# Kernel tuning notes

Hardware: AMD Instinct MI355X
Metric: run time of the kernel (lower is better)

## Reference

```python
import jax, jax.numpy as jnp
import numpy as np

N = 50000
E = 800000
IN = 64
HID = 64
OUT = 32
R = 8
B = 8
EPS = 1e-5


def setup_inputs() -> dict:
    key = jax.random.key(0)
    ks = jax.random.split(key, 20)
    s_in = 1.0 / np.sqrt(IN)
    s_hid = 1.0 / np.sqrt(HID)
    inp = {
        "x": jax.random.normal(ks[0], (N, IN), dtype=jnp.float32),
        "edge_index": jax.random.randint(ks[1], (2, E), 0, N, dtype=jnp.int64) if jax.config.jax_enable_x64 else jax.random.randint(ks[1], (2, E), 0, N),
        "edge_type": jax.random.randint(ks[2], (E,), 0, R),
        # conv1: in -> hid
        "comp1": jax.random.normal(ks[3], (R, B), dtype=jnp.float32) * (1.0 / np.sqrt(B)),
        "bases1": jax.random.normal(ks[4], (B, IN, HID), dtype=jnp.float32) * s_in,
        "root1": jax.random.normal(ks[5], (IN, HID), dtype=jnp.float32) * s_in,
        "bias1": jnp.zeros((HID,), dtype=jnp.float32),
        # conv2 (hidden): hid -> hid
        "comp2": jax.random.normal(ks[6], (R, B), dtype=jnp.float32) * (1.0 / np.sqrt(B)),
        "bases2": jax.random.normal(ks[7], (B, HID, HID), dtype=jnp.float32) * s_hid,
        "root2": jax.random.normal(ks[8], (HID, HID), dtype=jnp.float32) * s_hid,
        "bias2": jnp.zeros((HID,), dtype=jnp.float32),
        # conv_out: hid -> out
        "comp3": jax.random.normal(ks[9], (R, B), dtype=jnp.float32) * (1.0 / np.sqrt(B)),
        "bases3": jax.random.normal(ks[10], (B, HID, OUT), dtype=jnp.float32) * s_hid,
        "root3": jax.random.normal(ks[11], (HID, OUT), dtype=jnp.float32) * s_hid,
        "bias3": jnp.zeros((OUT,), dtype=jnp.float32),
        # batchnorms
        "gamma1": jnp.ones((HID,), dtype=jnp.float32),
        "beta1": jnp.zeros((HID,), dtype=jnp.float32),
        "gamma2": jnp.ones((HID,), dtype=jnp.float32),
        "beta2": jnp.zeros((HID,), dtype=jnp.float32),
    }
    return inp


def rgcn_conv(x, src, dst, etype, comp, bases, root, bias):
    """PyG-style RGCNConv with basis decomposition and per-relation mean aggregation."""
    n = x.shape[0]
    # project node features through all bases: [N, B, O]
    xb = jnp.einsum('ni,bio->nbo', x, bases)
    # per-edge relation coefficients [E, B] contract with gathered basis features [E, B, O]
    msg = jnp.einsum('eb,ebo->eo', comp[etype], xb[src])
    # mean normalization per (dst node, relation)
    seg = dst * R + etype
    cnt = jax.ops.segment_sum(jnp.ones((msg.shape[0],), dtype=x.dtype), seg, num_segments=n * R)
    msg = msg / jnp.maximum(cnt[seg], 1.0)[:, None]
    agg = jax.ops.segment_sum(msg, dst, num_segments=n)
    return agg + x @ root + bias


def batch_norm(x, gamma, beta):
    mu = jnp.mean(x, axis=0)
    var = jnp.mean(jnp.square(x - mu), axis=0)  # biased, as torch BN training
    return (x - mu) * jax.lax.rsqrt(var + EPS) * gamma + beta


def reference(x, edge_index, edge_type, comp1, bases1, root1, bias1,
              comp2, bases2, root2, bias2, comp3, bases3, root3, bias3,
              gamma1, beta1, gamma2, beta2):
    src, dst = edge_index[0], edge_index[1]
    h = rgcn_conv(x, src, dst, edge_type, comp1, bases1, root1, bias1)
    h = batch_norm(jax.nn.relu(h), gamma1, beta1)  # dropout = identity (eval)
    h_res = h  # residual since in_channels == hidden_channels
    h2 = rgcn_conv(h, src, dst, edge_type, comp2, bases2, root2, bias2)
    h2 = batch_norm(jax.nn.relu(h2), gamma2, beta2)
    h = h2 + h_res
    out = rgcn_conv(h, src, dst, edge_type, comp3, bases3, root3, bias3)
    return out
```

## Files before the change

kernel.cpp:

```cpp
#include <hip/hip_runtime.h>

#define NN 50000
#define NE 800000
#define RR 8
#define BB 8
#define EPSV 1e-5f
#define SCAN_B ((NN + 255) / 256)

typedef unsigned short bfu;
typedef __attribute__((ext_vector_type(8))) short bf16x8;
typedef __attribute__((ext_vector_type(4))) float f32x4;

__device__ inline float bf2f(bfu u) { return __uint_as_float(((unsigned)u) << 16); }
__device__ inline bfu f2bf(float f) {
    unsigned u = __float_as_uint(f);
    return (bfu)((u + 0x7fffu + ((u >> 16) & 1u)) >> 16);
}

__global__ void zero_f32(float* __restrict__ p, long n) {
    long i = (long)blockIdx.x * blockDim.x + threadIdx.x;
    long stride = (long)gridDim.x * blockDim.x;
    for (; i < n; i += stride) p[i] = 0.f;
}

__global__ void cvt_bf16(const float* __restrict__ x, bfu* __restrict__ xb, long n) {
    long i = (long)blockIdx.x * blockDim.x + threadIdx.x;
    long stride = (long)gridDim.x * blockDim.x;
    for (; i < n; i += stride) xb[i] = f2bf(x[i]);
}

__global__ void build_w_packed(const float* __restrict__ comp, const float* __restrict__ bases,
                               const float* __restrict__ root, bfu* __restrict__ Wp, int O) {
    int idx = blockIdx.x * blockDim.x + threadIdx.x;
    int tot = 576 * O;
    if (idx >= tot) return;
    int k = idx / O, o = idx % O;
    float val;
    if (k < 512) {
        int r = k >> 6, i = k & 63;
        val = 0.f;
#pragma unroll
        for (int b = 0; b < BB; ++b)
            val += comp[r * BB + b] * bases[(b * 64 + i) * O + o];
    } else {
        val = root[(k - 512) * O + o];
    }
    int kt = k >> 5, kk = k & 31;
    int lane = ((kk >> 3) << 4) | (o & 15);
    int pos = ((kt * (O / 16) + (o >> 4)) * 64 + lane) * 8 + (kk & 7);
    Wp[pos] = f2bf(val);
}

__global__ void edge_count(const int* __restrict__ ei, const int* __restrict__ et,
                           float* __restrict__ cnt) {
    int i = blockIdx.x * blockDim.x + threadIdx.x;
    int stride = gridDim.x * blockDim.x;
    for (int e = i; e < NE; e += stride) {
        int d = ei[NE + e];
        int r = et[e];
        atomicAdd(&cnt[(size_t)d * RR + r], 1.0f);
    }
}

__global__ void scan1(const float* __restrict__ cnt, int* __restrict__ offs, int* __restrict__ bsum) {
    __shared__ int sh[256];
    int b = blockIdx.x, t = threadIdx.x;
    int i = b * 256 + t;
    int v = 0;
    if (i < NN) {
        float s = 0.f;
#pragma unroll
        for (int r = 0; r < RR; ++r) s += cnt[(size_t)i * RR + r];
        v = (int)s;
    }
    sh[t] = v;
    __syncthreads();
    for (int s = 1; s < 256; s <<= 1) {
        int tmp = (t >= s) ? sh[t - s] : 0;
        __syncthreads();
        sh[t] += tmp;
        __syncthreads();
    }
    if (i < NN) offs[i] = sh[t] - v;
    if (t == 255) bsum[b] = sh[255];
}

__global__ void scan2(int* __restrict__ bsum, int* __restrict__ offs) {
    if (threadIdx.x == 0 && blockIdx.x == 0) {
        int run = 0;
        for (int b = 0; b < SCAN_B; ++b) { int t = bsum[b]; bsum[b] = run; run += t; }
        offs[NN] = run;
    }
}

__global__ void scan3(int* __restrict__ offs, const int* __restrict__ bsum) {
    int b = blockIdx.x, t = threadIdx.x;
    int i = b * 256 + t;
    if (i < NN) offs[i] += bsum[b];
}

__global__ void place(const int* __restrict__ ei, const int* __restrict__ et,
                      const int* __restrict__ offs, int* __restrict__ fill,
                      unsigned* __restrict__ esrt) {
    int i = blockIdx.x * blockDim.x + threadIdx.x;
    int stride = gridDim.x * blockDim.x;
    for (int e = i; e < NE; e += stride) {
        int d = ei[NE + e];
        int pos = offs[d] + atomicAdd(&fill[d], 1);
        esrt[pos] = ((unsigned)ei[e] << 3) | (unsigned)et[e];
    }
}

#define ACCUM(U, V)                                              \
    switch (__builtin_amdgcn_readfirstlane((int)((U) & 7u))) {   \
        case 0: a0 += (V); break;                                \
        case 1: a1 += (V); break;                                \
        case 2: a2 += (V); break;                                \
        case 3: a3 += (V); break;                                \
        case 4: a4 += (V); break;                                \
        case 5: a5 += (V); break;                                \
        case 6: a6 += (V); break;                                \
        default: a7 += (V); break;                               \
    }

template <int O, bool RELU>
__global__ __launch_bounds__(256) void agg_gemm(const int* __restrict__ offs,
                                                const unsigned* __restrict__ esrt,
                                                const float* __restrict__ cnt,
                                                const bfu* __restrict__ xb,
                                                const bfu* __restrict__ Wp,
                                                const float* __restrict__ bias,
                                                float* __restrict__ outp) {
    constexpr int CT = O / 16;
    __shared__ bfu Af[1152 * 8];
    int wave = threadIdx.x >> 6, lane = threadIdx.x & 63;
    int n0 = blockIdx.x * 16;
    int c = lane;
    int swz_lo = ((c >> 3) & 3) << 4;

#pragma unroll 1
    for (int i = 0; i < 4; ++i) {
        int row = wave * 4 + i;
        int n = n0 + row;
        int j0 = offs[n], j1 = offs[n + 1];
        float a0 = 0.f, a1 = 0.f, a2 = 0.f, a3 = 0.f, a4 = 0.f, a5 = 0.f, a6 = 0.f, a7 = 0.f;
        int j = j0;
        for (; j + 4 <= j1; j += 4) {
            unsigned u0 = esrt[j], u1 = esrt[j + 1], u2 = esrt[j + 2], u3 = esrt[j + 3];
            float v0 = bf2f(xb[(size_t)(u0 >> 3) * 64 + lane]);
            float v1 = bf2f(xb[(size_t)(u1 >> 3) * 64 + lane]);
            float v2 = bf2f(xb[(size_t)(u2 >> 3) * 64 + lane]);
            float v3 = bf2f(xb[(size_t)(u3 >> 3) * 64 + lane]);
            ACCUM(u0, v0); ACCUM(u1, v1); ACCUM(u2, v2); ACCUM(u3, v3);
        }
        for (; j < j1; ++j) {
            unsigned u = esrt[j];
            float v = bf2f(xb[(size_t)(u >> 3) * 64 + lane]);
            ACCUM(u, v);
        }
#define WR(r, ar) {                                                            \
        float inv = 1.f / fmaxf(cnt[(size_t)n * RR + (r)], 1.f);               \
        bfu bv = f2bf((ar) * inv);                                             \
        int g = (2 * (r) + (c >> 5)) * 64 + (row | swz_lo);                    \
        int gs = g ^ ((g >> 3) & 7) ^ ((g >> 6) & 7);                          \
        Af[gs * 8 + (c & 7)] = bv; }
        WR(0, a0) WR(1, a1) WR(2, a2) WR(3, a3)
        WR(4, a4) WR(5, a5) WR(6, a6) WR(7, a7)
#undef WR
        {
            bfu bv = xb[(size_t)n * 64 + lane];
            int g = (16 + (c >> 5)) * 64 + (row | swz_lo);
            int gs = g ^ ((g >> 3) & 7) ^ ((g >> 6) & 7);
            Af[gs * 8 + (c & 7)] = bv;
        }
    }
    __syncthreads();

    int ct = wave;
    if (CT == 4 || ct < CT) {
        f32x4 acc = (f32x4){0.f, 0.f, 0.f, 0.f};
#pragma unroll
        for (int kt = 0; kt < 18; ++kt) {
            int g = kt * 64 + lane;
            int gs = g ^ ((g >> 3) & 7) ^ ((g >> 6) & 7);
            bf16x8 af = *(const bf16x8*)&Af[gs * 8];
            bf16x8 bfv = *(const bf16x8*)&Wp[((size_t)(kt * CT + ct) * 64 + lane) * 8];
            acc = __builtin_amdgcn_mfma_f32_16x16x32_bf16(af, bfv, acc, 0, 0, 0);
        }
        int col = ct * 16 + (lane & 15);
        float b = bias[col];
#pragma unroll
        for (int jj = 0; jj < 4; ++jj) {
            int row = (lane >> 4) * 4 + jj;
            float v = acc[jj] + b;
            if (RELU) v = fmaxf(v, 0.f);
            outp[(size_t)(n0 + row) * O + col] = v;
        }
    }
}

__global__ void bn_stats(const float* __restrict__ y, float* __restrict__ stats) {
    int c = threadIdx.x & 63;
    int rg = threadIdx.x >> 6;
    float s = 0.f, q = 0.f;
    for (int n = blockIdx.x * 4 + rg; n < NN; n += gridDim.x * 4) {
        float v = y[(size_t)n * 64 + c];
        s += v;
        q += v * v;
    }
    __shared__ float ls[4][64], lq[4][64];
    ls[rg][c] = s;
    lq[rg][c] = q;
    __syncthreads();
    if (rg == 0) {
        s = ls[0][c] + ls[1][c] + ls[2][c] + ls[3][c];
        q = lq[0][c] + lq[1][c] + lq[2][c] + lq[3][c];
        atomicAdd(&stats[c], s);
        atomicAdd(&stats[64 + c], q);
    }
}

__global__ void bn_finalize(const float* __restrict__ stats, const float* __restrict__ gamma,
                            const float* __restrict__ beta, float* __restrict__ sc) {
    int c = threadIdx.x;
    if (c < 64) {
        float mu = stats[c] / (float)NN;
        float var = stats[64 + c] / (float)NN - mu * mu;
        float scale = gamma[c] * rsqrtf(var + EPSV);
        sc[c] = scale;
        sc[64 + c] = beta[c] - mu * scale;
    }
}

__global__ void bn_apply(const float* __restrict__ y, const float* __restrict__ sc,
                         const bfu* __restrict__ resb, bfu* __restrict__ hb) {
    long tot = (long)NN * 64;
    long stride = (long)gridDim.x * blockDim.x;
    for (long i = (long)blockIdx.x * blockDim.x + threadIdx.x; i < tot; i += stride) {
        int c = (int)(i & 63);
        float v = y[i] * sc[c] + sc[64 + c];
        if (resb) v += bf2f(resb[i]);
        hb[i] = f2bf(v);
    }
}

extern "C" void kernel_launch(void* const* d_in, const int* in_sizes, int n_in,
                              void* d_out, int out_size, void* d_ws, size_t ws_size,
                              hipStream_t stream) {
    const float* x      = (const float*)d_in[0];
    const int*   ei     = (const int*)d_in[1];
    const int*   et     = (const int*)d_in[2];
    const float* comp1  = (const float*)d_in[3];
    const float* bases1 = (const float*)d_in[4];
    const float* root1  = (const float*)d_in[5];
    const float* bias1  = (const float*)d_in[6];
    const float* comp2  = (const float*)d_in[7];
    const float* bases2 = (const float*)d_in[8];
    const float* root2  = (const float*)d_in[9];
    const float* bias2  = (const float*)d_in[10];
    const float* comp3  = (const float*)d_in[11];
    const float* bases3 = (const float*)d_in[12];
    const float* root3  = (const float*)d_in[13];
    const float* bias3  = (const float*)d_in[14];
    const float* gamma1 = (const float*)d_in[15];
    const float* beta1  = (const float*)d_in[16];
    const float* gamma2 = (const float*)d_in[17];
    const float* beta2  = (const float*)d_in[18];
    float* out = (float*)d_out;

    float* ws = (float*)d_ws;
    size_t off = 0;
    bfu* Wp1 = (bfu*)(ws + off); off += 18432;
    bfu* Wp2 = (bfu*)(ws + off); off += 18432;
    bfu* Wp3 = (bfu*)(ws + off); off += 9216;
    float* stats = ws + off; off += 128;
    float* sc = ws + off; off += 128;
    float* cnt = ws + off; off += (size_t)NN * RR;
    float* y  = ws + off; off += (size_t)NN * 64;
    bfu* xb   = (bfu*)(ws + off); off += (size_t)NN * 32;
    bfu* h1b  = (bfu*)(ws + off); off += (size_t)NN * 32;
    bfu* hb   = (bfu*)(ws + off); off += (size_t)NN * 32;
    int* offs = (int*)(ws + off); off += NN + 4;
    int* fill = (int*)(ws + off); off += NN;
    int* bsum = (int*)(ws + off); off += 256;
    unsigned* esrt = (unsigned*)(ws + off); off += NE;

    build_w_packed<<<dim3((576 * 64 + 255) / 256), dim3(256), 0, stream>>>(comp1, bases1, root1, Wp1, 64);
    build_w_packed<<<dim3((576 * 64 + 255) / 256), dim3(256), 0, stream>>>(comp2, bases2, root2, Wp2, 64);
    build_w_packed<<<dim3((576 * 32 + 255) / 256), dim3(256), 0, stream>>>(comp3, bases3, root3, Wp3, 32);
    cvt_bf16<<<dim3(512), dim3(256), 0, stream>>>(x, xb, (long)NN * 64);
    zero_f32<<<dim3(512), dim3(256), 0, stream>>>(cnt, (long)NN * RR);
    zero_f32<<<dim3(128), dim3(256), 0, stream>>>((float*)fill, NN);
    edge_count<<<dim3(1024), dim3(256), 0, stream>>>(ei, et, cnt);
    scan1<<<dim3(SCAN_B), dim3(256), 0, stream>>>(cnt, offs, bsum);
    scan2<<<dim3(1), dim3(64), 0, stream>>>(bsum, offs);
    scan3<<<dim3(SCAN_B), dim3(256), 0, stream>>>(offs, bsum);
    place<<<dim3(1024), dim3(256), 0, stream>>>(ei, et, offs, fill, esrt);

    agg_gemm<64, true><<<dim3(NN / 16), dim3(256), 0, stream>>>(offs, esrt, cnt, xb, Wp1, bias1, y);
    zero_f32<<<dim3(1), dim3(128), 0, stream>>>(stats, 128);
    bn_stats<<<dim3(256), dim3(256), 0, stream>>>(y, stats);
    bn_finalize<<<dim3(1), dim3(64), 0, stream>>>(stats, gamma1, beta1, sc);
    bn_apply<<<dim3(1024), dim3(256), 0, stream>>>(y, sc, nullptr, h1b);

    agg_gemm<64, true><<<dim3(NN / 16), dim3(256), 0, stream>>>(offs, esrt, cnt, h1b, Wp2, bias2, y);
    zero_f32<<<dim3(1), dim3(128), 0, stream>>>(stats, 128);
    bn_stats<<<dim3(256), dim3(256), 0, stream>>>(y, stats);
    bn_finalize<<<dim3(1), dim3(64), 0, stream>>>(stats, gamma2, beta2, sc);
    bn_apply<<<dim3(1024), dim3(256), 0, stream>>>(y, sc, h1b, hb);

    agg_gemm<32, false><<<dim3(NN / 16), dim3(256), 0, stream>>>(offs, esrt, cnt, hb, Wp3, bias3, out);
}
```

Baseline: 345.6 us.

## Fuse prep kernels, fold BN stats into GEMM, partition edge atomics by range

Several init kernels (weight packing, bf16 conversion, zeroing of counts, fill and stats) are merged into one prep kernel. BN statistics are now accumulated inside agg_gemm through grouped atomics, and the finalize step moves into bn_apply, which removes separate stats and finalize launches and an extra pass over y. edge_count and place split the grid into 8 destination ranges so each block's atomics hit a smaller address window, at the cost of every block scanning all edges. The gather loop is unrolled to 8 with scalar readfirstlane edge indices to expose more loads in flight.

Measured after the change: 290.9 us. 15.8% less time.

```diff
diff --git a/kernel.cpp b/kernel.cpp
--- a/kernel.cpp
+++ b/kernel.cpp
@@ -6,6 +6,7 @@
 #define BB 8
 #define EPSV 1e-5f
 #define SCAN_B ((NN + 255) / 256)
+#define NGRP 64
 
 typedef unsigned short bfu;
 typedef __attribute__((ext_vector_type(8))) short bf16x8;
@@ -17,23 +18,15 @@
     return (bfu)((u + 0x7fffu + ((u >> 16) & 1u)) >> 16);
 }
 
-__global__ void zero_f32(float* __restrict__ p, long n) {
-    long i = (long)blockIdx.x * blockDim.x + threadIdx.x;
-    long stride = (long)gridDim.x * blockDim.x;
-    for (; i < n; i += stride) p[i] = 0.f;
-}
-
-__global__ void cvt_bf16(const float* __restrict__ x, bfu* __restrict__ xb, long n) {
-    long i = (long)blockIdx.x * blockDim.x + threadIdx.x;
-    long stride = (long)gridDim.x * blockDim.x;
-    for (; i < n; i += stride) xb[i] = f2bf(x[i]);
-}
-
-__global__ void build_w_packed(const float* __restrict__ comp, const float* __restrict__ bases,
-                               const float* __restrict__ root, bfu* __restrict__ Wp, int O) {
-    int idx = blockIdx.x * blockDim.x + threadIdx.x;
-    int tot = 576 * O;
-    if (idx >= tot) return;
+#define NW1 36864L
+#define NW2 36864L
+#define NW3 18432L
+#define NCV ((long)NN * 64)
+#define NZ  (400000L + 50000L + 2L * NGRP * 128)
+
+__device__ inline void build_one(const float* __restrict__ comp, const float* __restrict__ bases,
+                                 const float* __restrict__ root, bfu* __restrict__ Wp,
+                                 int O, int idx) {
     int k = idx / O, o = idx % O;
     float val;
     if (k < 512) {
@@ -51,14 +44,35 @@
     Wp[pos] = f2bf(val);
 }
 
+__global__ void prep(const float* __restrict__ c1, const float* __restrict__ b1,
+                     const float* __restrict__ r1, bfu* __restrict__ Wp1,
+                     const float* __restrict__ c2, const float* __restrict__ b2,
+                     const float* __restrict__ r2, bfu* __restrict__ Wp2,
+                     const float* __restrict__ c3, const float* __restrict__ b3,
+                     const float* __restrict__ r3, bfu* __restrict__ Wp3,
+                     const float* __restrict__ x, bfu* __restrict__ xb,
+                     float* __restrict__ zbase) {
+    long i = (long)blockIdx.x * blockDim.x + threadIdx.x;
+    long stride = (long)gridDim.x * blockDim.x;
+    const long tot = NW1 + NW2 + NW3 + NCV + NZ;
+    for (; i < tot; i += stride) {
+        if (i < NW1) build_one(c1, b1, r1, Wp1, 64, (int)i);
+        else if (i < NW1 + NW2) build_one(c2, b2, r2, Wp2, 64, (int)(i - NW1));
+        else if (i < NW1 + NW2 + NW3) build_one(c3, b3, r3, Wp3, 32, (int)(i - NW1 - NW2));
+        else if (i < NW1 + NW2 + NW3 + NCV) { long k = i - NW1 - NW2 - NW3; xb[k] = f2bf(x[k]); }
+        else zbase[i - (NW1 + NW2 + NW3 + NCV)] = 0.f;
+    }
+}
+
 __global__ void edge_count(const int* __restrict__ ei, const int* __restrict__ et,
                            float* __restrict__ cnt) {
-    int i = blockIdx.x * blockDim.x + threadIdx.x;
-    int stride = gridDim.x * blockDim.x;
-    for (int e = i; e < NE; e += stride) {
+    int range = blockIdx.x >> 8;
+    int lo = range * (NN / 8), hi = lo + NN / 8;
+    int i = (blockIdx.x & 255) * 256 + threadIdx.x;
+    for (int e = i; e < NE; e += 256 * 256) {
         int d = ei[NE + e];
-        int r = et[e];
-        atomicAdd(&cnt[(size_t)d * RR + r], 1.0f);
+        if (d >= lo && d < hi)
+            atomicAdd(&cnt[(size_t)d * RR + et[e]], 1.0f);
     }
 }
 
@@ -102,35 +116,41 @@
 __global__ void place(const int* __restrict__ ei, const int* __restrict__ et,
                       const int* __restrict__ offs, int* __restrict__ fill,
                       unsigned* __restrict__ esrt) {
-    int i = blockIdx.x * blockDim.x + threadIdx.x;
-    int stride = gridDim.x * blockDim.x;
-    for (int e = i; e < NE; e += stride) {
+    int range = blockIdx.x >> 8;
+    int lo = range * (NN / 8), hi = lo + NN / 8;
+    int i = (blockIdx.x & 255) * 256 + threadIdx.x;
+    for (int e = i; e < NE; e += 256 * 256) {
         int d = ei[NE + e];
-        int pos = offs[d] + atomicAdd(&fill[d], 1);
-        esrt[pos] = ((unsigned)ei[e] << 3) | (unsigned)et[e];
-    }
-}
-
-#define ACCUM(U, V)                                              \
-    switch (__builtin_amdgcn_readfirstlane((int)((U) & 7u))) {   \
-        case 0: a0 += (V); break;                                \
-        case 1: a1 += (V); break;                                \
-        case 2: a2 += (V); break;                                \
-        case 3: a3 += (V); break;                                \
-        case 4: a4 += (V); break;                                \
-        case 5: a5 += (V); break;                                \
-        case 6: a6 += (V); break;                                \
-        default: a7 += (V); break;                               \
-    }
-
-template <int O, bool RELU>
+        if (d >= lo && d < hi) {
+            int pos = offs[d] + atomicAdd(&fill[d], 1);
+            esrt[pos] = ((unsigned)ei[e] << 3) | (unsigned)et[e];
+        }
+    }
+}
+
+#define ACCUMS(SU, V)                          \
+    switch ((SU) & 7) {                        \
+        case 0: a0 += (V); break;              \
+        case 1: a1 += (V); break;              \
+        case 2: a2 += (V); break;              \
+        case 3: a3 += (V); break;              \
+        case 4: a4 += (V); break;              \
+        case 5: a5 += (V); break;              \
+        case 6: a6 += (V); break;              \
+        default: a7 += (V); break;             \
+    }
+#define RFL(X) __builtin_amdgcn_readfirstlane((int)(X))
+#define GATH(S) bf2f(xb[((size_t)((unsigned)(S) >> 3)) * 64 + lane])
+
+template <int O, bool RELU, bool STATS>
 __global__ __launch_bounds__(256) void agg_gemm(const int* __restrict__ offs,
                                                 const unsigned* __restrict__ esrt,
                                                 const float* __restrict__ cnt,
                                                 const bfu* __restrict__ xb,
                                                 const bfu* __restrict__ Wp,
                                                 const float* __restrict__ bias,
-                                                float* __restrict__ outp) {
+                                                float* __restrict__ outp,
+                                                float* __restrict__ stats) {
     constexpr int CT = O / 16;
     __shared__ bfu Af[1152 * 8];
     int wave = threadIdx.x >> 6, lane = threadIdx.x & 63;
@@ -145,18 +165,26 @@
         int j0 = offs[n], j1 = offs[n + 1];
         float a0 = 0.f, a1 = 0.f, a2 = 0.f, a3 = 0.f, a4 = 0.f, a5 = 0.f, a6 = 0.f, a7 = 0.f;
         int j = j0;
+        for (; j + 8 <= j1; j += 8) {
+            int s0 = RFL(esrt[j + 0]), s1 = RFL(esrt[j + 1]);
+            int s2 = RFL(esrt[j + 2]), s3 = RFL(esrt[j + 3]);
+            int s4 = RFL(esrt[j + 4]), s5 = RFL(esrt[j + 5]);
+            int s6 = RFL(esrt[j + 6]), s7 = RFL(esrt[j + 7]);
+            float v0 = GATH(s0), v1 = GATH(s1), v2 = GATH(s2), v3 = GATH(s3);
+            float v4 = GATH(s4), v5 = GATH(s5), v6 = GATH(s6), v7 = GATH(s7);
+            ACCUMS(s0, v0) ACCUMS(s1, v1) ACCUMS(s2, v2) ACCUMS(s3, v3)
+            ACCUMS(s4, v4) ACCUMS(s5, v5) ACCUMS(s6, v6) ACCUMS(s7, v7)
+        }
         for (; j + 4 <= j1; j += 4) {
-            unsigned u0 = esrt[j], u1 = esrt[j + 1], u2 = esrt[j + 2], u3 = esrt[j + 3];
-            float v0 = bf2f(xb[(size_t)(u0 >> 3) * 64 + lane]);
-            float v1 = bf2f(xb[(size_t)(u1 >> 3) * 64 + lane]);
-            float v2 = bf2f(xb[(size_t)(u2 >> 3) * 64 + lane]);
-            float v3 = bf2f(xb[(size_t)(u3 >> 3) * 64 + lane]);
-            ACCUM(u0, v0); ACCUM(u1, v1); ACCUM(u2, v2); ACCUM(u3, v3);
+            int s0 = RFL(esrt[j + 0]), s1 = RFL(esrt[j + 1]);
+            int s2 = RFL(esrt[j + 2]), s3 = RFL(esrt[j + 3]);
+            float v0 = GATH(s0), v1 = GATH(s1), v2 = GATH(s2), v3 = GATH(s3);
+            ACCUMS(s0, v0) ACCUMS(s1, v1) ACCUMS(s2, v2) ACCUMS(s3, v3)
         }
         for (; j < j1; ++j) {
-            unsigned u = esrt[j];
-            float v = bf2f(xb[(size_t)(u >> 3) * 64 + lane]);
-            ACCUM(u, v);
+            int s0 = RFL(esrt[j]);
+            float v0 = GATH(s0);
+            ACCUMS(s0, v0)
         }
 #define WR(r, ar) {                                                            \
         float inv = 1.f / fmaxf(cnt[(size_t)n * RR + (r)], 1.f);               \
@@ -189,57 +217,55 @@
         }
         int col = ct * 16 + (lane & 15);
         float b = bias[col];
+        float ssum = 0.f, sq = 0.f;
 #pragma unroll
         for (int jj = 0; jj < 4; ++jj) {
             int row = (lane >> 4) * 4 + jj;
             float v = acc[jj] + b;
             if (RELU) v = fmaxf(v, 0.f);
             outp[(size_t)(n0 + row) * O + col] = v;
-        }
-    }
-}
-
-__global__ void bn_stats(const float* __restrict__ y, float* __restrict__ stats) {
-    int c = threadIdx.x & 63;
-    int rg = threadIdx.x >> 6;
-    float s = 0.f, q = 0.f;
-    for (int n = blockIdx.x * 4 + rg; n < NN; n += gridDim.x * 4) {
-        float v = y[(size_t)n * 64 + c];
-        s += v;
-        q += v * v;
-    }
-    __shared__ float ls[4][64], lq[4][64];
-    ls[rg][c] = s;
-    lq[rg][c] = q;
+            if (STATS) { ssum += v; sq += v * v; }
+        }
+        if (STATS) {
+            ssum += __shfl_xor(ssum, 16); ssum += __shfl_xor(ssum, 32);
+            sq   += __shfl_xor(sq, 16);   sq   += __shfl_xor(sq, 32);
+            if ((lane >> 4) == 0) {
+                int g = blockIdx.x & (NGRP - 1);
+                atomicAdd(&stats[g * 128 + col], ssum);
+                atomicAdd(&stats[g * 128 + 64 + col], sq);
+            }
+        }
+    }
+}
+
+template <bool HASRES>
+__global__ __launch_bounds__(256) void bn_apply(const float* __restrict__ y,
+                                                const float* __restrict__ stats,
+                                                const float* __restrict__ gamma,
+                                                const float* __restrict__ beta,
+                                                const bfu* __restrict__ resb,
+                                                bfu* __restrict__ hb) {
+    __shared__ float sc[128];
+    int t = threadIdx.x;
+    if (t < 64) {
+        float s = 0.f, q = 0.f;
+        for (int g = 0; g < NGRP; ++g) {
+            s += stats[g * 128 + t];
+            q += stats[g * 128 + 64 + t];
+        }
+        float mu = s / (float)NN;
+        float var = q / (float)NN - mu * mu;
+        float scale = gamma[t] * rsqrtf(var + EPSV);
+        sc[t] = scale;
+        sc[64 + t] = beta[t] - mu * scale;
+    }
     __syncthreads();
-    if (rg == 0) {
-        s = ls[0][c] + ls[1][c] + ls[2][c] + ls[3][c];
-        q = lq[0][c] + lq[1][c] + lq[2][c] + lq[3][c];
-        atomicAdd(&stats[c], s);
-        atomicAdd(&stats[64 + c], q);
-    }
-}
-
-__global__ void bn_finalize(const float* __restrict__ stats, const float* __restrict__ gamma,
-                            const float* __restrict__ beta, float* __restrict__ sc) {
-    int c = threadIdx.x;
-    if (c < 64) {
-        float mu = stats[c] / (float)NN;
-        float var = stats[64 + c] / (float)NN - mu * mu;
-        float scale = gamma[c] * rsqrtf(var + EPSV);
-        sc[c] = scale;
-        sc[64 + c] = beta[c] - mu * scale;
-    }
-}
-
-__global__ void bn_apply(const float* __restrict__ y, const float* __restrict__ sc,
-                         const bfu* __restrict__ resb, bfu* __restrict__ hb) {
     long tot = (long)NN * 64;
     long stride = (long)gridDim.x * blockDim.x;
     for (long i = (long)blockIdx.x * blockDim.x + threadIdx.x; i < tot; i += stride) {
-        int c = (int)(i & 63);
-        float v = y[i] * sc[c] + sc[64 + c];
-        if (resb) v += bf2f(resb[i]);
+        int cc = (int)(i & 63);
+        float v = y[i] * sc[cc] + sc[64 + cc];
+        if (HASRES) v += bf2f(resb[i]);
         hb[i] = f2bf(v);
     }
 }
@@ -258,10 +284,10 @@
     const float* bases2 = (const float*)d_in[8];
     const float* root2  = (const float*)d_in[9];
     const float* bias2  = (const float*)d_in[10];
+    const float* bias3  = (const float*)d_in[14];
     const float* comp3  = (const float*)d_in[11];
     const float* bases3 = (const float*)d_in[12];
     const float* root3  = (const float*)d_in[13];
-    const float* bias3  = (const float*)d_in[14];
     const float* gamma1 = (const float*)d_in[15];
     const float* beta1  = (const float*)d_in[16];
     const float* gamma2 = (const float*)d_in[17];
@@ -273,41 +299,33 @@
     bfu* Wp1 = (bfu*)(ws + off); off += 18432;
     bfu* Wp2 = (bfu*)(ws + off); off += 18432;
     bfu* Wp3 = (bfu*)(ws + off); off += 9216;
-    float* stats = ws + off; off += 128;
-    float* sc = ws + off; off += 128;
-    float* cnt = ws + off; off += (size_t)NN * RR;
+    float* cnt    = ws + off; off += (size_t)NN * RR;
+    int*   fill   = (int*)(ws + off); off += NN;
+    float* stats1 = ws + off; off += NGRP * 128;
+    float* stats2 = ws + off; off += NGRP * 128;
     float* y  = ws + off; off += (size_t)NN * 64;
     bfu* xb   = (bfu*)(ws + off); off += (size_t)NN * 32;
     bfu* h1b  = (bfu*)(ws + off); off += (size_t)NN * 32;
     bfu* hb   = (bfu*)(ws + off); off += (size_t)NN * 32;
     int* offs = (int*)(ws + off); off += NN + 4;
-    int* fill = (int*)(ws + off); off += NN;
     int* bsum = (int*)(ws + off); off += 256;
     unsigned* esrt = (unsigned*)(ws + off); off += NE;
 
-    build_w_packed<<<dim3((576 * 64 + 255) / 256), dim3(256), 0, stream>>>(comp1, bases1, root1, Wp1, 64);
-    build_w_packed<<<dim3((576 * 64 + 255) / 256), dim3(256), 0, stream>>>(comp2, bases2, root2, Wp2, 64);
-    build_w_packed<<<dim3((576 * 32 + 255) / 256), dim3(256), 0, stream>>>(comp3, bases3, root3, Wp3, 32);
-    cvt_bf16<<<dim3(512), dim3(256), 0, stream>>>(x, xb, (long)NN * 64);
-    zero_f32<<<dim3(512), dim3(256), 0, stream>>>(cnt, (long)NN * RR);
-    zero_f32<<<dim3(128), dim3(256), 0, stream>>>((float*)fill, NN);
-    edge_count<<<dim3(1024), dim3(256), 0, stream>>>(ei, et, cnt);
+    prep<<<dim3(2048), dim3(256), 0, stream>>>(comp1, bases1, root1, Wp1,
+                                               comp2, bases2, root2, Wp2,
+                                               comp3, bases3, root3, Wp3,
+                                               x, xb, cnt);
+    edge_count<<<dim3(2048), dim3(256), 0, stream>>>(ei, et, cnt);
     scan1<<<dim3(SCAN_B), dim3(256), 0, stream>>>(cnt, offs, bsum);
     scan2<<<dim3(1), dim3(64), 0, stream>>>(bsum, offs);
     scan3<<<dim3(SCAN_B), dim3(256), 0, stream>>>(offs, bsum);
-    place<<<dim3(1024), dim3(256), 0, stream>>>(ei, et, offs, fill, esrt);
-
-    agg_gemm<64, true><<<dim3(NN / 16), dim3(256), 0, stream>>>(offs, esrt, cnt, xb, Wp1, bias1, y);
-    zero_f32<<<dim3(1), dim3(128), 0, stream>>>(stats, 128);
-    bn_stats<<<dim3(256), dim3(256), 0, stream>>>(y, stats);
-    bn_finalize<<<dim3(1), dim3(64), 0, stream>>>(stats, gamma1, beta1, sc);
-    bn_apply<<<dim3(1024), dim3(256), 0, stream>>>(y, sc, nullptr, h1b);
-
-    agg_gemm<64, true><<<dim3(NN / 16), dim3(256), 0, stream>>>(offs, esrt, cnt, h1b, Wp2, bias2, y);
-    zero_f32<<<dim3(1), dim3(128), 0, stream>>>(stats, 128);
-    bn_stats<<<dim3(256), dim3(256), 0, stream>>>(y, stats);
-    bn_finalize<<<dim3(1), dim3(64), 0, stream>>>(stats, gamma2, beta2, sc);
-    bn_apply<<<dim3(1024), dim3(256), 0, stream>>>(y, sc, h1b, hb);
-
-    agg_gemm<32, false><<<dim3(NN / 16), dim3(256), 0, stream>>>(offs, esrt, cnt, hb, Wp3, bias3, out);
-}
+    place<<<dim3(2048), dim3(256), 0, stream>>>(ei, et, offs, fill, esrt);
+
+    agg_gemm<64, true, true><<<dim3(NN / 16), dim3(256), 0, stream>>>(offs, esrt, cnt, xb, Wp1, bias1, y, stats1);
+    bn_apply<false><<<dim3(256), dim3(256), 0, stream>>>(y, stats1, gamma1, beta1, nullptr, h1b);
+
+    agg_gemm<64, true, true><<<dim3(NN / 16), dim3(256), 0, stream>>>(offs, esrt, cnt, h1b, Wp2, bias2, y, stats2);
+    bn_apply<true><<<dim3(256), dim3(256), 0, stream>>>(y, stats2, gamma2, beta2, h1b, hb);
+
+    agg_gemm<32, false, false><<<dim3(NN / 16), dim3(256), 0, stream>>>(offs, esrt, cnt, hb, Wp3, bias3, out, nullptr);
+}
```
